# Kernel optimization log

Hardware: AMD Instinct MI355X
Metric: run time of the kernel (lower is better)

## Reference

```python
import jax, jax.numpy as jnp
import numpy as np

NGRAM_NS = (2, 3)  # window sizes of the 2 hidden layers ('2,3,4' -> num_hidden_layers=2)


def _ngram(x, n):
    # x: (b, s, d) -> (b, s, n, d); window i holds x[i:i+n], zero-padded at the end
    s = x.shape[1]
    xp = jnp.pad(x, ((0, 0), (0, n - 1), (0, 0)))
    return jnp.stack([xp[:, j:j + s] for j in range(n)], axis=2)


def _mixture_weighted(r, i, w):
    # r,i: (..., n, d); w: (..., n, 1) -> weighted sum of outer products |phi><phi|
    w = w[..., 0]
    Rr = jnp.einsum('...nd,...ne,...n->...de', r, r, w) + jnp.einsum('...nd,...ne,...n->...de', i, i, w)
    Ri = jnp.einsum('...nd,...ne,...n->...de', i, r, w) - jnp.einsum('...nd,...ne,...n->...de', r, i, w)
    return Rr, Ri


def _normalize_complex(vr, vi):
    n = jnp.sqrt(jnp.sum(vr * vr + vi * vi, axis=-1, keepdims=True))
    return vr / n, vi / n


def _quad_form(Rr, Ri, vr, vi):
    # <v_k| rho |v_k> for each measurement vector v_k; Rr,Ri: (..., d, d); vr,vi: (k, d)
    ar = jnp.einsum('...de,ke->...dk', Rr, vr) - jnp.einsum('...de,ke->...dk', Ri, vi)
    ai = jnp.einsum('...de,ke->...dk', Rr, vi) + jnp.einsum('...de,ke->...dk', Ri, vr)
    out_r = jnp.einsum('kd,...dk->...k', vr, ar) + jnp.einsum('kd,...dk->...k', vi, ai)
    out_i = jnp.einsum('kd,...dk->...k', vr, ai) - jnp.einsum('kd,...dk->...k', vi, ar)
    return out_r, out_i


def setup_inputs() -> dict:
    key = jax.random.key(0)
    ks = jax.random.split(key, 9)
    V, D, B, S, U, L = 50000, 100, 16, 128, 100, 2
    return {
        'input_seq': jax.random.randint(ks[0], (B, S), 0, V),
        'amp_table': jax.random.normal(ks[1], (V, D), jnp.float32),
        'phase_table': jax.random.uniform(ks[2], (V, D), jnp.float32, -np.pi, np.pi),
        'proj_kernel_r': jax.random.normal(ks[3], (L, D, D), jnp.float32),
        'proj_kernel_i': jax.random.normal(ks[4], (L, D, D), jnp.float32),
        'meas_kernel_r': jax.random.normal(ks[5], (U, D), jnp.float32),
        'meas_kernel_i': jax.random.normal(ks[6], (U, D), jnp.float32),
        'dense_w': jax.random.normal(ks[7], (U, 2), jnp.float32) * 0.1,
        'dense_b': jnp.zeros((2,), jnp.float32),
    }


def reference(input_seq, amp_table, phase_table, proj_kernel_r, proj_kernel_i,
              meas_kernel_r, meas_kernel_i, dense_w, dense_b):
    # ComplexEmbedding
    amp = amp_table[input_seq]      # (b, s, d)
    phase = phase_table[input_seq]  # (b, s, d)
    # L2Norm / L2Normalization
    weights = jnp.linalg.norm(amp, axis=-1, keepdims=True)  # (b, s, 1)
    amp = amp / weights
    # ComplexMultiply: state = amp * e^{i phase}
    seq_r = amp * jnp.cos(phase)
    seq_i = amp * jnp.sin(phase)
    for li, n in enumerate(NGRAM_NS):
        gr = _ngram(seq_r, n)                                  # (b, s, n, d)
        gi = _ngram(seq_i, n)
        gw = jax.nn.softmax(_ngram(weights, n), axis=1)        # Softmax(dim=1) as in torch code
        Rr, Ri = _mixture_weighted(gr, gi, gw)                 # (b, s, d, d)
        vr, vi = _normalize_complex(proj_kernel_r[li], proj_kernel_i[li])
        seq_r, seq_i = _quad_form(Rr, Ri, vr, vi)              # (b, s, d)
    # Final mixture over the sequence dim with the raw L2-norm weights
    Rr, Ri = _mixture_weighted(seq_r, seq_i, weights)          # (b, d, d)
    vr, vi = _normalize_complex(meas_kernel_r, meas_kernel_i)
    probs, _ = _quad_form(Rr, Ri, vr, vi)                      # (b, units) real part of Tr(rho P_k)
    return probs @ dense_w + dense_b
```

## Files before the change

### kernel.cpp

```cpp
#include <hip/hip_runtime.h>
#include <math.h>

#define NB 16
#define SS 128
#define DD 100
#define KK 100
#define T_TILE 8
#define P_HALO 11
#define NTILES 16
#define NT 768
#define NWAVES 12
#define CH_D4 5
#define NCHUNK 5

__device__ __forceinline__ float dot4(const float4 a, const float4 b) {
  return a.x * b.x + a.y * b.y + a.z * b.z + a.w * b.w;
}

__device__ __forceinline__ void ld_chunk(const float* __restrict__ gvr,
                                         const float* __restrict__ gvi,
                                         int c, int tid,
                                         float4& pv0, float4& pv1) {
  const int e0 = tid;
  const int p0 = e0 / 500, rm0 = e0 % 500, r0_ = rm0 / 100, k0_ = rm0 % 100;
  pv0 = *(const float4*)((p0 ? gvi : gvr) + k0_ * DD + 4 * (CH_D4 * c + r0_));
  const int e1 = tid + NT;
  if (e1 < 1000) {
    const int p1 = e1 / 500, rm1 = e1 % 500, r1_ = rm1 / 100, k1_ = rm1 % 100;
    pv1 = *(const float4*)((p1 ? gvi : gvr) + k1_ * DD + 4 * (CH_D4 * c + r1_));
  }
}
__device__ __forceinline__ void st_chunk(float4 (*__restrict__ vt)[1000],
                                         int buf, int tid,
                                         const float4& pv0, const float4& pv1) {
  vt[buf][tid] = pv0;
  if (tid + NT < 1000) vt[buf][tid + NT] = pv1;
}

template<int MODE>
__device__ __forceinline__ void accum_pair(
    const float4* __restrict__ vtb,
    const float4 (*__restrict__ bxr)[25], const float4 (*__restrict__ bxi)[25],
    int p0, int p1, bool a0, bool a1, int k, int c,
    float& r0a, float& i0a, float& r1a, float& i1a, float& n0)
{
#pragma unroll
  for (int r = 0; r < CH_D4; ++r) {
    const int d4 = c * CH_D4 + r;
    const float4 vr4 = vtb[r * KK + k];
    const float4 vi4 = vtb[500 + r * KK + k];
    n0 += dot4(vr4, vr4) + dot4(vi4, vi4);
    if (a0) {
      const float4 x4 = bxr[p0][d4];
      if (MODE == 0) {
        const float4 z4 = bxi[p0][d4];
        r0a += dot4(vr4, x4) + dot4(vi4, z4);
        i0a += dot4(vr4, z4) - dot4(vi4, x4);
      } else {
        r0a += dot4(vr4, x4);
        i0a += dot4(vi4, x4);
      }
    }
    if (a1) {
      const float4 x4 = bxr[p1][d4];
      if (MODE == 0) {
        const float4 z4 = bxi[p1][d4];
        r1a += dot4(vr4, x4) + dot4(vi4, z4);
        i1a += dot4(vr4, z4) - dot4(vi4, x4);
      } else {
        r1a += dot4(vr4, x4);
        i1a += dot4(vi4, x4);
      }
    }
  }
}

template<int MODE>
__device__ __forceinline__ void run_stage(
    const float* __restrict__ gvr, const float* __restrict__ gvi,
    const float* __restrict__ gnr, const float* __restrict__ gni,
    float4 (*__restrict__ vt)[1000],
    const float4 (*__restrict__ bxr)[25], const float4 (*__restrict__ bxi)[25],
    float* __restrict__ mflat, float2* __restrict__ y2flat,
    float* __restrict__ invvn, const int nslots,
    const int tid, const int lane, const int wid,
    float4& pv0, float4& pv1)
{
  st_chunk(vt, 0, tid, pv0, pv1);
  __syncthreads();

  const int s0 = wid, s1 = wid + NWAVES;
  float a0r = 0.f, a0i = 0.f, a1r = 0.f, a1i = 0.f, n0 = 0.f;
  const int kk = (s0 & 1) * 50 + lane;
  const int pp0 = s0 >> 1, pp1 = s1 >> 1;
  const bool act0 = (s0 < nslots), act1 = (s1 < nslots);

  for (int c = 0; c < NCHUNK; ++c) {
    const int buf = c & 1;
    if (c + 1 < NCHUNK)  ld_chunk(gvr, gvi, c + 1, tid, pv0, pv1);
    else if (gnr)        ld_chunk(gnr, gni, 0,     tid, pv0, pv1);
    if (lane < 50)
      accum_pair<MODE>(vt[buf], bxr, bxi, pp0, pp1, act0, act1, kk, c,
                       a0r, a0i, a1r, a1i, n0);
    if (c + 1 < NCHUNK)
      st_chunk(vt, buf ^ 1, tid, pv0, pv1);
    __syncthreads();
  }

  if (lane < 50) {
    const float rcp = 1.0f / n0;
    if (act0) {
      if (MODE == 0) mflat[pp0 * KK + kk] = (a0r * a0r + a0i * a0i) * rcp;
      else           y2flat[pp0 * KK + kk] = make_float2(a0r, a0i);
    }
    if (act1) {
      if (MODE == 0) mflat[pp1 * KK + kk] = (a1r * a1r + a1i * a1i) * rcp;
      else           y2flat[pp1 * KK + kk] = make_float2(a1r, a1i);
    }
    if (wid < 2) invvn[kk] = rcp;
  }
}

__global__ __launch_bounds__(NT) void k_fused(
    const int* __restrict__ seq,
    const float* __restrict__ ampT, const float* __restrict__ phT,
    const float* __restrict__ pkr, const float* __restrict__ pki,
    const float* __restrict__ mkr, const float* __restrict__ mki,
    float* __restrict__ part)
{
  __shared__ float4 vt[2][1000];
  __shared__ float4 xr4[P_HALO][25];
  __shared__ float4 xi4[P_HALO][25];
  __shared__ float4 m4[P_HALO][25];
  __shared__ float2 y2[P_HALO][KK];
  __shared__ float es[SS];
  __shared__ float wnl[SS];
  __shared__ float invvn[KK];
  __shared__ float redw[NWAVES];
  __shared__ float sc[3];

  const int tid  = threadIdx.x;
  const int lane = tid & 63;
  const int wid  = tid >> 6;
  const int bt   = blockIdx.x;
  const int b    = bt >> 4;
  const int tile = bt & 15;
  const int t0   = tile * T_TILE;
  const int sb   = b * SS;

  float4 pv0, pv1;
  ld_chunk(pkr, pki, 0, tid, pv0, pv1);

  if (tid < 4 * SS) {
    const int t = tid >> 2, q = tid & 3;
    const int row = seq[sb + t];
    const float* ap = ampT + (long)row * DD + q;
    float s = 0.f;
#pragma unroll
    for (int i = 0; i < 25; ++i) { const float a = ap[4*i]; s += a * a; }
    s += __shfl_xor(s, 1, 64);
    s += __shfl_xor(s, 2, 64);
    if (q == 0) { const float nrm = sqrtf(s); wnl[t] = nrm; es[t] = expf(nrm); }
  }
  __syncthreads();

  {
    float v = (tid < SS) ? es[tid] : 0.f;
    for (int m = 32; m; m >>= 1) v += __shfl_xor(v, m, 64);
    if (lane == 0) redw[wid] = v;
  }
  for (int idx = tid; idx < P_HALO * 25; idx += NT) {
    const int p = idx / 25, d4 = idx % 25;
    const int tp = t0 + p;
    float4 o_r = {0.f, 0.f, 0.f, 0.f}, o_i = {0.f, 0.f, 0.f, 0.f};
    if (tp < SS) {
      const int row = seq[sb + tp];
      const float4 a4 = *(const float4*)(ampT + (long)row * DD + 4 * d4);
      const float4 p4 = *(const float4*)(phT  + (long)row * DD + 4 * d4);
      const float inv = 1.0f / wnl[tp];
      float sv, cv;
      sincosf(p4.x, &sv, &cv); o_r.x = a4.x * inv * cv; o_i.x = a4.x * inv * sv;
      sincosf(p4.y, &sv, &cv); o_r.y = a4.y * inv * cv; o_i.y = a4.y * inv * sv;
      sincosf(p4.z, &sv, &cv); o_r.z = a4.z * inv * cv; o_i.z = a4.z * inv * sv;
      sincosf(p4.w, &sv, &cv); o_r.w = a4.w * inv * cv; o_i.w = a4.w * inv * sv;
    }
    xr4[p][d4] = o_r;
    xi4[p][d4] = o_i;
  }
  __syncthreads();
  if (tid == 0) {
    float E = 0.f;
    for (int w = 0; w < NWAVES; ++w) E += redw[w];
    sc[0] = E;
    sc[1] = E - es[0] + 1.0f;
    sc[2] = E - es[0] - es[1] + 2.0f;
  }
  __syncthreads();

  run_stage<0>(pkr, pki, pkr + DD * DD, pki + DD * DD, vt, xr4, xi4,
               (float*)m4, nullptr, invvn, 2 * P_HALO,
               tid, lane, wid, pv0, pv1);
  __syncthreads();

  run_stage<1>(pkr + DD * DD, pki + DD * DD, mkr, mki, vt, m4, m4,
               nullptr, (float2*)y2, invvn, 2 * P_HALO,
               tid, lane, wid, pv0, pv1);
  __syncthreads();

  {
    const float E = sc[0], Z1 = sc[1];
    for (int idx = tid; idx < 10 * KK; idx += NT) {
      const int p = idx / KK, k = idx - p * KK;
      const int t = t0 + p;
      const float w0 = ((t     < SS) ? es[t]     : 1.f) / E;
      const float w1 = ((t + 1 < SS) ? es[t + 1] : 1.f) / Z1;
      const float2 ya = y2[p][k], yb = y2[p + 1][k];
      const float ar = w0 * ya.x + w1 * yb.x;
      const float ai = w0 * ya.y + w1 * yb.y;
      ((float*)m4)[p * KK + k] = (ar * ar + ai * ai) * invvn[k];
    }
  }
  __syncthreads();

  run_stage<1>(mkr, mki, nullptr, nullptr, vt, m4, m4,
               nullptr, (float2*)y2, invvn, 20,
               tid, lane, wid, pv0, pv1);
  __syncthreads();

  {
    const float E = sc[0], Z1 = sc[1], Z2 = sc[2];
    for (int idx = tid; idx < T_TILE * KK; idx += NT) {
      const int p = idx / KK, k = idx - p * KK;
      const int t = t0 + p;
      const float w0 = es[t] / E;
      const float w1 = ((t + 1 < SS) ? es[t + 1] : 1.f) / Z1;
      const float w2 = ((t + 2 < SS) ? es[t + 2] : 1.f) / Z2;
      const float2 ya = y2[p][k], yb = y2[p + 1][k], yc = y2[p + 2][k];
      const float qr = w0 * ya.x + w1 * yb.x + w2 * yc.x;
      const float qi = w0 * ya.y + w1 * yb.y + w2 * yc.y;
      ((float*)m4)[p * KK + k] = wnl[t] * (qr * qr + qi * qi) * invvn[k];
    }
  }
  __syncthreads();
  if (tid < KK) {
    float s = 0.f;
#pragma unroll
    for (int p = 0; p < T_TILE; ++p) s += ((float*)m4)[p * KK + tid];
    part[bt * KK + tid] = s;
  }
}

__global__ __launch_bounds__(128) void k_out(
    const float* __restrict__ part, const float* __restrict__ dw,
    const float* __restrict__ db, float* __restrict__ out)
{
  __shared__ float pr[KK];
  const int b = blockIdx.x, tid = threadIdx.x;
  if (tid < KK) {
    float s = 0.f;
#pragma unroll
    for (int q = 0; q < NTILES; ++q) s += part[(b * NTILES + q) * KK + tid];
    pr[tid] = s;
  }
  __syncthreads();
  if (tid < 2) {
    float s = db[tid];
    for (int k = 0; k < KK; ++k) s += pr[k] * dw[k * 2 + tid];
    out[b * 2 + tid] = s;
  }
}

extern "C" void kernel_launch(void* const* d_in, const int* in_sizes, int n_in,
                              void* d_out, int out_size, void* d_ws, size_t ws_size,
                              hipStream_t stream) {
  const int*   seq  = (const int*)d_in[0];
  const float* ampT = (const float*)d_in[1];
  const float* phT  = (const float*)d_in[2];
  const float* pkr  = (const float*)d_in[3];
  const float* pki  = (const float*)d_in[4];
  const float* mkr  = (const float*)d_in[5];
  const float* mki  = (const float*)d_in[6];
  const float* dw   = (const float*)d_in[7];
  const float* db   = (const float*)d_in[8];
  float* out  = (float*)d_out;
  float* part = (float*)d_ws;

  k_fused<<<NB * NTILES, NT, 0, stream>>>(seq, ampT, phT, pkr, pki, mkr, mki, part);
  k_out  <<<NB,          128, 0, stream>>>(part, dw, db, out);
}
```

Baseline: 34.20 us.

## Route stage inputs through global memory and scalar loads instead of LDS

The intermediate activations of stage one and the sequence-mixed stage-two activations are now written to a per-block global scratch buffer. Later stages read them back with inline s_load_dwordx16/x4 scalar loads into SGPRs, so the per-wave x operand is uniform and no longer comes from shared memory. The wave id is made uniform with readfirstlane. This cuts LDS read traffic in the inner dot-product loops. In exchange it adds a global write and read-back path, relies on the scalar cache being coherent with vector stores through __syncthreads without an explicit invalidate, and adds manual lgkmcnt waits.

```diff
diff --git a/kernel.cpp b/kernel.cpp
--- a/kernel.cpp
+++ b/kernel.cpp
@@ -12,9 +12,19 @@
 #define NWAVES 12
 #define CH_D4 5
 #define NCHUNK 5
+#define XROWF 128
+
+typedef float sf16 __attribute__((ext_vector_type(16)));
+typedef float sf4  __attribute__((ext_vector_type(4)));
 
 __device__ __forceinline__ float dot4(const float4 a, const float4 b) {
   return a.x * b.x + a.y * b.y + a.z * b.z + a.w * b.w;
+}
+
+__device__ __forceinline__ void sl20(const float* p, sf16& a, sf4& b) {
+  asm volatile("s_load_dwordx16 %0, %2, 0x0\n\t"
+               "s_load_dwordx4  %1, %2, 0x40"
+               : "=s"(a), "=s"(b) : "s"((unsigned long long)p));
 }
 
 __device__ __forceinline__ void ld_chunk(const float* __restrict__ gvr,
@@ -37,8 +47,7 @@
   if (tid + NT < 1000) vt[buf][tid + NT] = pv1;
 }
 
-template<int MODE>
-__device__ __forceinline__ void accum_pair(
+__device__ __forceinline__ void accum_pair0(
     const float4* __restrict__ vtb,
     const float4 (*__restrict__ bxr)[25], const float4 (*__restrict__ bxi)[25],
     int p0, int p1, bool a0, bool a1, int k, int c,
@@ -52,41 +61,68 @@
     n0 += dot4(vr4, vr4) + dot4(vi4, vi4);
     if (a0) {
       const float4 x4 = bxr[p0][d4];
-      if (MODE == 0) {
-        const float4 z4 = bxi[p0][d4];
-        r0a += dot4(vr4, x4) + dot4(vi4, z4);
-        i0a += dot4(vr4, z4) - dot4(vi4, x4);
-      } else {
-        r0a += dot4(vr4, x4);
-        i0a += dot4(vi4, x4);
-      }
+      const float4 z4 = bxi[p0][d4];
+      r0a += dot4(vr4, x4) + dot4(vi4, z4);
+      i0a += dot4(vr4, z4) - dot4(vi4, x4);
     }
     if (a1) {
       const float4 x4 = bxr[p1][d4];
-      if (MODE == 0) {
-        const float4 z4 = bxi[p1][d4];
-        r1a += dot4(vr4, x4) + dot4(vi4, z4);
-        i1a += dot4(vr4, z4) - dot4(vi4, x4);
-      } else {
-        r1a += dot4(vr4, x4);
-        i1a += dot4(vi4, x4);
-      }
-    }
-  }
-}
-
-template<int MODE>
-__device__ __forceinline__ void run_stage(
+      const float4 z4 = bxi[p1][d4];
+      r1a += dot4(vr4, x4) + dot4(vi4, z4);
+      i1a += dot4(vr4, z4) - dot4(vi4, x4);
+    }
+  }
+}
+
+__device__ __forceinline__ void run_stage1(
     const float* __restrict__ gvr, const float* __restrict__ gvi,
     const float* __restrict__ gnr, const float* __restrict__ gni,
     float4 (*__restrict__ vt)[1000],
     const float4 (*__restrict__ bxr)[25], const float4 (*__restrict__ bxi)[25],
-    float* __restrict__ mflat, float2* __restrict__ y2flat,
-    float* __restrict__ invvn, const int nslots,
+    float* __restrict__ m1g,
     const int tid, const int lane, const int wid,
     float4& pv0, float4& pv1)
 {
   st_chunk(vt, 0, tid, pv0, pv1);
+  __syncthreads();
+
+  const int s0 = wid, s1 = wid + NWAVES;
+  float a0r = 0.f, a0i = 0.f, a1r = 0.f, a1i = 0.f, n0 = 0.f;
+  const int kk = (s0 & 1) * 50 + lane;
+  const int pp0 = s0 >> 1, pp1 = s1 >> 1;
+  const bool act0 = (s0 < 2 * P_HALO), act1 = (s1 < 2 * P_HALO);
+
+  for (int c = 0; c < NCHUNK; ++c) {
+    const int buf = c & 1;
+    if (c + 1 < NCHUNK) ld_chunk(gvr, gvi, c + 1, tid, pv0, pv1);
+    else                ld_chunk(gnr, gni, 0,     tid, pv0, pv1);
+    if (lane < 50)
+      accum_pair0(vt[buf], bxr, bxi, pp0, pp1, act0, act1, kk, c,
+                  a0r, a0i, a1r, a1i, n0);
+    if (c + 1 < NCHUNK) st_chunk(vt, buf ^ 1, tid, pv0, pv1);
+    __syncthreads();
+  }
+
+  if (lane < 50) {
+    const float rcp = 1.0f / n0;
+    if (act0) m1g[pp0 * XROWF + kk] = (a0r * a0r + a0i * a0i) * rcp;
+    if (act1) m1g[pp1 * XROWF + kk] = (a1r * a1r + a1i * a1i) * rcp;
+  }
+}
+
+__device__ __forceinline__ void run_stage_sx(
+    const float* __restrict__ gvr, const float* __restrict__ gvi,
+    const float* __restrict__ gnr, const float* __restrict__ gni,
+    const float* __restrict__ xrow0, const float* __restrict__ xrow1,
+    float4 (*__restrict__ vt)[1000],
+    float2* __restrict__ y2flat, float* __restrict__ invvn, const int nslots,
+    const int tid, const int lane, const int wid,
+    float4& pv0, float4& pv1)
+{
+  st_chunk(vt, 0, tid, pv0, pv1);
+  sf16 xa0, xa1; sf4 xb0, xb1;
+  sl20(xrow0, xa0, xb0);
+  sl20(xrow1, xa1, xb1);
   __syncthreads();
 
   const int s0 = wid, s1 = wid + NWAVES;
@@ -97,26 +133,47 @@
 
   for (int c = 0; c < NCHUNK; ++c) {
     const int buf = c & 1;
+    asm volatile("s_waitcnt lgkmcnt(0)"
+                 : "+s"(xa0), "+s"(xb0), "+s"(xa1), "+s"(xb1));
     if (c + 1 < NCHUNK)  ld_chunk(gvr, gvi, c + 1, tid, pv0, pv1);
     else if (gnr)        ld_chunk(gnr, gni, 0,     tid, pv0, pv1);
-    if (lane < 50)
-      accum_pair<MODE>(vt[buf], bxr, bxi, pp0, pp1, act0, act1, kk, c,
-                       a0r, a0i, a1r, a1i, n0);
-    if (c + 1 < NCHUNK)
+    if (lane < 50) {
+      const float4* vtb = vt[buf];
+#pragma unroll
+      for (int r = 0; r < CH_D4; ++r) {
+        const float4 vr4 = vtb[r * KK + kk];
+        const float4 vi4 = vtb[500 + r * KK + kk];
+        n0 += dot4(vr4, vr4) + dot4(vi4, vi4);
+        float x00, x01, x02, x03, x10, x11, x12, x13;
+        if (r < 4) {
+          x00 = xa0[4*r+0]; x01 = xa0[4*r+1]; x02 = xa0[4*r+2]; x03 = xa0[4*r+3];
+          x10 = xa1[4*r+0]; x11 = xa1[4*r+1]; x12 = xa1[4*r+2]; x13 = xa1[4*r+3];
+        } else {
+          x00 = xb0[0]; x01 = xb0[1]; x02 = xb0[2]; x03 = xb0[3];
+          x10 = xb1[0]; x11 = xb1[1]; x12 = xb1[2]; x13 = xb1[3];
+        }
+        if (act0) {
+          a0r += vr4.x * x00 + vr4.y * x01 + vr4.z * x02 + vr4.w * x03;
+          a0i += vi4.x * x00 + vi4.y * x01 + vi4.z * x02 + vi4.w * x03;
+        }
+        if (act1) {
+          a1r += vr4.x * x10 + vr4.y * x11 + vr4.z * x12 + vr4.w * x13;
+          a1i += vi4.x * x10 + vi4.y * x11 + vi4.z * x12 + vi4.w * x13;
+        }
+      }
+    }
+    if (c + 1 < NCHUNK) {
+      sl20(xrow0 + 20 * (c + 1), xa0, xb0);
+      sl20(xrow1 + 20 * (c + 1), xa1, xb1);
       st_chunk(vt, buf ^ 1, tid, pv0, pv1);
+    }
     __syncthreads();
   }
 
   if (lane < 50) {
     const float rcp = 1.0f / n0;
-    if (act0) {
-      if (MODE == 0) mflat[pp0 * KK + kk] = (a0r * a0r + a0i * a0i) * rcp;
-      else           y2flat[pp0 * KK + kk] = make_float2(a0r, a0i);
-    }
-    if (act1) {
-      if (MODE == 0) mflat[pp1 * KK + kk] = (a1r * a1r + a1i * a1i) * rcp;
-      else           y2flat[pp1 * KK + kk] = make_float2(a1r, a1i);
-    }
+    if (act0) y2flat[pp0 * KK + kk] = make_float2(a0r, a0i);
+    if (act1) y2flat[pp1 * KK + kk] = make_float2(a1r, a1i);
     if (wid < 2) invvn[kk] = rcp;
   }
 }
@@ -126,7 +183,7 @@
     const float* __restrict__ ampT, const float* __restrict__ phT,
     const float* __restrict__ pkr, const float* __restrict__ pki,
     const float* __restrict__ mkr, const float* __restrict__ mki,
-    float* __restrict__ part)
+    float* __restrict__ M1, float* __restrict__ M2, float* __restrict__ part)
 {
   __shared__ float4 vt[2][1000];
   __shared__ float4 xr4[P_HALO][25];
@@ -141,12 +198,15 @@
 
   const int tid  = threadIdx.x;
   const int lane = tid & 63;
-  const int wid  = tid >> 6;
+  const int wid  = __builtin_amdgcn_readfirstlane(tid >> 6);
   const int bt   = blockIdx.x;
   const int b    = bt >> 4;
   const int tile = bt & 15;
   const int t0   = tile * T_TILE;
   const int sb   = b * SS;
+
+  float* m1g = M1 + bt * (P_HALO * XROWF);
+  float* m2g = M2 + bt * (10 * XROWF);
 
   float4 pv0, pv1;
   ld_chunk(pkr, pki, 0, tid, pv0, pv1);
@@ -197,14 +257,17 @@
   }
   __syncthreads();
 
-  run_stage<0>(pkr, pki, pkr + DD * DD, pki + DD * DD, vt, xr4, xi4,
-               (float*)m4, nullptr, invvn, 2 * P_HALO,
-               tid, lane, wid, pv0, pv1);
-  __syncthreads();
-
-  run_stage<1>(pkr + DD * DD, pki + DD * DD, mkr, mki, vt, m4, m4,
-               nullptr, (float2*)y2, invvn, 2 * P_HALO,
-               tid, lane, wid, pv0, pv1);
+  run_stage1(pkr, pki, pkr + DD * DD, pki + DD * DD, vt, xr4, xi4,
+             m1g, tid, lane, wid, pv0, pv1);
+  __syncthreads();
+
+  {
+    const int pp0 = wid >> 1, pp1 = (wid + NWAVES) >> 1;
+    const float* xr0 = m1g + min(pp0, P_HALO - 1) * XROWF;
+    const float* xr1 = m1g + min(pp1, P_HALO - 1) * XROWF;
+    run_stage_sx(pkr + DD * DD, pki + DD * DD, mkr, mki, xr0, xr1, vt,
+                 (float2*)y2, invvn, 2 * P_HALO, tid, lane, wid, pv0, pv1);
+  }
   __syncthreads();
 
   {
@@ -217,14 +280,18 @@
       const float2 ya = y2[p][k], yb = y2[p + 1][k];
       const float ar = w0 * ya.x + w1 * yb.x;
       const float ai = w0 * ya.y + w1 * yb.y;
-      ((float*)m4)[p * KK + k] = (ar * ar + ai * ai) * invvn[k];
-    }
-  }
-  __syncthreads();
-
-  run_stage<1>(mkr, mki, nullptr, nullptr, vt, m4, m4,
-               nullptr, (float2*)y2, invvn, 20,
-               tid, lane, wid, pv0, pv1);
+      m2g[p * XROWF + k] = (ar * ar + ai * ai) * invvn[k];
+    }
+  }
+  __syncthreads();
+
+  {
+    const int pp0 = wid >> 1, pp1 = (wid + NWAVES) >> 1;
+    const float* xr0 = m2g + min(pp0, 9) * XROWF;
+    const float* xr1 = m2g + min(pp1, 9) * XROWF;
+    run_stage_sx(mkr, mki, nullptr, nullptr, xr0, xr1, vt,
+                 (float2*)y2, invvn, 20, tid, lane, wid, pv0, pv1);
+  }
   __syncthreads();
 
   {
@@ -282,9 +349,14 @@
   const float* mki  = (const float*)d_in[6];
   const float* dw   = (const float*)d_in[7];
   const float* db   = (const float*)d_in[8];
-  float* out  = (float*)d_out;
-  float* part = (float*)d_ws;
-
-  k_fused<<<NB * NTILES, NT, 0, stream>>>(seq, ampT, phT, pkr, pki, mkr, mki, part);
+  float* out = (float*)d_out;
+
+  float* ws   = (float*)d_ws;
+  float* part = ws;
+  float* M1   = ws + 25600;
+  float* M2   = M1 + 256 * P_HALO * XROWF;
+
+  k_fused<<<NB * NTILES, NT, 0, stream>>>(seq, ampT, phT, pkr, pki, mkr, mki,
+                                          M1, M2, part);
   k_out  <<<NB,          128, 0, stream>>>(part, dw, db, out);
 }
```

After: 35.47 us. 1.04x slower.
